# Performance work log

Hardware: AMD Instinct MI355X
Metric: run time of the kernel (lower is better)

Reference implementation:

```python
import jax, jax.numpy as jnp
import numpy as np

N = 100000      # nodes
E = 1200000     # edges (avg degree ~12)
D_IN = 64
D_OUT = 64


def setup_inputs() -> dict:
    key = jax.random.key(0)
    k1, k2, k3, k4 = jax.random.split(key, 4)
    x = jax.random.normal(k1, (N, D_IN), dtype=jnp.float32)
    # learned params (glorot-ish init)
    W = jax.random.normal(k2, (D_IN, D_OUT), dtype=jnp.float32) / np.sqrt(D_IN).astype(np.float32)
    b = jnp.zeros((D_OUT,), dtype=jnp.float32)
    src = jax.random.randint(k3, (E,), 0, N, dtype=jnp.int32)
    dst = jax.random.randint(k4, (E,), 0, N, dtype=jnp.int32)
    return {"x": x, "W": W, "b": b, "src": src, "dst": dst}


def reference(x, W, b, src, dst):
    # GCN layer: h = relu( D^-1/2 A D^-1/2 (x @ W) + b ), dropout=0 (eval)
    ones = jnp.ones(src.shape[0], dtype=x.dtype)
    deg_out = jax.ops.segment_sum(ones, src, num_segments=N)   # out-degree of source nodes
    deg_in = jax.ops.segment_sum(ones, dst, num_segments=N)    # in-degree of dest nodes
    norm_src = jax.lax.rsqrt(jnp.maximum(deg_out, 1.0))
    norm_dst = jax.lax.rsqrt(jnp.maximum(deg_in, 1.0))

    h = x @ W                                                  # [N, D_OUT] dense transform
    msg = h[src] * norm_src[src][:, None]                      # [E, D_OUT] gathered, pre-normalized messages
    agg = jax.ops.segment_sum(msg, dst, num_segments=N)        # [N, D_OUT] sparse aggregation
    out = agg * norm_dst[:, None] + b
    return jax.nn.relu(out)
```

## Files before the change

kernel.cpp:

```cpp
#include <hip/hip_runtime.h>
#include <hip/hip_bf16.h>

#define N_NODES 100000
#define N_EDGES 1200000
#define NPAIRS  (N_EDGES / 2)
#define DCH 64

#define K1B 256
#define K1T 1024
#define NRID 8
#define RID_NODES 12500
#define RID_WORDS 3125
#define SLICE_PAIRS (NPAIRS / (K1B / NRID))
#define SCAT_PAIRS ((NPAIRS + K1B - 1) / K1B)

#define BNODES 128
#define KBUK ((N_NODES + BNODES - 1) / BNODES)
#define CAPE 3008
#define CAPN 40

#define K2B 256
#define K2T 1024
#define GW_TOT (K2B * K2T / 64)

#define K3T 512

#define OFF_DEG      0
#define OFF_GCUR     100096
#define OFF_FLAG     103296
#define OFF_ESORT    103424
#define OFF_HS       9512704

__device__ __forceinline__ float load_f(const void* p, int i, int f32) {
    if (f32) return ((const float*)p)[i];
    return __bfloat162float(((const __hip_bfloat16*)p)[i]);
}

__device__ __forceinline__ unsigned short f2bf_bits(float f) {
    __hip_bfloat16 h = __float2bfloat16(f);
    return __builtin_bit_cast(unsigned short, h);
}

__global__ __launch_bounds__(K1T, 4)
void edges_kernel(const int* __restrict__ src,
                  const int* __restrict__ dst,
                  const void* __restrict__ x,
                  unsigned int* __restrict__ deg_packed,
                  int* __restrict__ gcur,
                  unsigned int* __restrict__ esort,
                  int* __restrict__ flag) {
    __shared__ unsigned int h[RID_WORDS];
    __shared__ int cnt[KBUK];
    __shared__ int base[KBUK];
    __shared__ int cur[KBUK];
    int tid = threadIdx.x, bid = blockIdx.x;

    if (bid == 0) {
        if (tid == 0) h[0] = 0;
        __syncthreads();
        if (tid < 256) {
            const unsigned short* u = (const unsigned short*)x;
            int c = 0;
            for (int i = tid * 16; i < tid * 16 + 16; ++i) {
                unsigned short v = u[2 * i];
                int e = (v >> 7) & 0xFF;
                if (e >= 141) c++;
            }
            if (c) atomicAdd(&h[0], (unsigned int)c);
        }
        __syncthreads();
        if (tid == 0) *flag = (h[0] > 256) ? 1 : 0;
        __syncthreads();
    }

    {
        int rid = bid & (NRID - 1);
        int j   = bid >> 3;
        for (int w = tid; w < RID_WORDS; w += K1T) h[w] = 0;
        __syncthreads();
        int lo = rid * RID_NODES;
        const int2* s2 = (const int2*)src;
        int p0 = j * SLICE_PAIRS, p1 = p0 + SLICE_PAIRS;
        for (int p = p0 + tid; p < p1; p += K1T) {
            int2 sp = s2[p];
            int n0 = sp.x - lo, n1 = sp.y - lo;
            if ((unsigned)n0 < (unsigned)RID_NODES)
                atomicAdd(&h[n0 >> 2], 1u << ((n0 & 3) * 8));
            if ((unsigned)n1 < (unsigned)RID_NODES)
                atomicAdd(&h[n1 >> 2], 1u << ((n1 & 3) * 8));
        }
        __syncthreads();
        unsigned int* dp = deg_packed + rid * RID_WORDS;
        for (int w = tid; w < RID_WORDS; w += K1T) {
            unsigned int v = h[w];
            if (v) atomicAdd(&dp[w], v);
        }
    }

    {
        int p0 = bid * SCAT_PAIRS;
        int p1 = p0 + SCAT_PAIRS; if (p1 > NPAIRS) p1 = NPAIRS;
        const int2* s2 = (const int2*)src;
        const int2* d2 = (const int2*)dst;
        for (int i = tid; i < KBUK; i += K1T) { cnt[i] = 0; cur[i] = 0; }
        __syncthreads();
        for (int p = p0 + tid; p < p1; p += K1T) {
            int2 dp = d2[p];
            atomicAdd(&cnt[dp.x >> 7], 1);
            atomicAdd(&cnt[dp.y >> 7], 1);
        }
        __syncthreads();
        for (int i = tid; i < KBUK; i += K1T)
            if (cnt[i]) base[i] = atomicAdd(&gcur[i], cnt[i]);
        __syncthreads();
        for (int p = p0 + tid; p < p1; p += K1T) {
            int2 sp = s2[p];
            int2 dp = d2[p];
            int b0 = dp.x >> 7, b1 = dp.y >> 7;
            int pos0 = base[b0] + atomicAdd(&cur[b0], 1);
            if (pos0 < CAPE)
                esort[b0 * CAPE + pos0] =
                    (unsigned int)sp.x | ((unsigned int)(dp.x & 127) << 24);
            int pos1 = base[b1] + atomicAdd(&cur[b1], 1);
            if (pos1 < CAPE)
                esort[b1 * CAPE + pos1] =
                    (unsigned int)sp.y | ((unsigned int)(dp.y & 127) << 24);
        }
    }
}

__global__ __launch_bounds__(K2T, 4)
void gemm_kernel(const void* __restrict__ x,
                 const void* __restrict__ W,
                 const unsigned int* __restrict__ deg_packed,
                 __hip_bfloat16* __restrict__ hs) {
    __shared__ float wt[DCH * 68];
    __shared__ int sn;
    int tid = threadIdx.x, bid = blockIdx.x;

    if (tid == 0) sn = 0;
    __syncthreads();
    if (tid < 256) {
        const unsigned short* u = (const unsigned short*)x;
        int c = 0;
        for (int i = tid * 16; i < tid * 16 + 16; ++i) {
            unsigned short v = u[2 * i];
            int e = (v >> 7) & 0xFF;
            if (e >= 141) c++;
        }
        if (c) atomicAdd(&sn, c);
    }
    __syncthreads();
    int f32 = sn > 256;

    for (int i = tid; i < DCH * DCH; i += K2T) {
        int kk = i >> 6, cc = i & 63;
        wt[cc * 68 + kk] = load_f(W, i, f32);
    }
    __syncthreads();

    int lane = tid & 63;
    const float4* wrow = (const float4*)(wt + lane * 68);
    float wr[DCH];
#pragma unroll
    for (int kq = 0; kq < 16; ++kq) {
        float4 t = wrow[kq];
        wr[4 * kq + 0] = t.x; wr[4 * kq + 1] = t.y;
        wr[4 * kq + 2] = t.z; wr[4 * kq + 3] = t.w;
    }
#pragma unroll
    for (int kk = 0; kk < DCH; ++kk)
        asm volatile("" : "+v"(wr[kk]));

    int gw = (bid << 4) + (tid >> 6);
#define RLA(i) __int_as_float(__builtin_amdgcn_readlane(xiA, (i)))
#define RLB(i) __int_as_float(__builtin_amdgcn_readlane(xiB, (i)))
#define GRP(j) \
    a0 = fmaf(RLA(4*(j)+0), wr[4*(j)+0], a0); \
    a1 = fmaf(RLA(4*(j)+1), wr[4*(j)+1], a1); \
    a2 = fmaf(RLA(4*(j)+2), wr[4*(j)+2], a2); \
    a3 = fmaf(RLA(4*(j)+3), wr[4*(j)+3], a3); \
    c0 = fmaf(RLB(4*(j)+0), wr[4*(j)+0], c0); \
    c1 = fmaf(RLB(4*(j)+1), wr[4*(j)+1], c1); \
    c2 = fmaf(RLB(4*(j)+2), wr[4*(j)+2], c2); \
    c3 = fmaf(RLB(4*(j)+3), wr[4*(j)+3], c3);

    for (int node = gw; node < N_NODES; node += 2 * GW_TOT) {
        int nodeB = node + GW_TOT;
        int hasB = nodeB < N_NODES;
        float xvA = load_f(x, node * DCH + lane, f32);
        float xvB = hasB ? load_f(x, nodeB * DCH + lane, f32) : 0.0f;
        int xiA = __float_as_int(xvA);
        int xiB = __float_as_int(xvB);
        float a0 = 0.f, a1 = 0.f, a2 = 0.f, a3 = 0.f;
        float c0 = 0.f, c1 = 0.f, c2 = 0.f, c3 = 0.f;
        GRP(0)  GRP(1)  GRP(2)  GRP(3)
        GRP(4)  GRP(5)  GRP(6)  GRP(7)
        GRP(8)  GRP(9)  GRP(10) GRP(11)
        GRP(12) GRP(13) GRP(14) GRP(15)
        unsigned int dwA = deg_packed[node >> 2];
        float dgA = (float)((dwA >> ((node & 3) * 8)) & 0xFFu);
        float nrA = rsqrtf(fmaxf(dgA, 1.0f));
        hs[node * DCH + lane] = __float2bfloat16(((a0 + a1) + (a2 + a3)) * nrA);
        if (hasB) {
            unsigned int dwB = deg_packed[nodeB >> 2];
            float dgB = (float)((dwB >> ((nodeB & 3) * 8)) & 0xFFu);
            float nrB = rsqrtf(fmaxf(dgB, 1.0f));
            hs[nodeB * DCH + lane] = __float2bfloat16(((c0 + c1) + (c2 + c3)) * nrB);
        }
    }
#undef RLA
#undef RLB
#undef GRP
}

__global__ __launch_bounds__(K3T, 6)
void gather_kernel(const __hip_bfloat16* __restrict__ hs,
                   const unsigned int* __restrict__ esort,
                   const int* __restrict__ gcur,
                   const void* __restrict__ b,
                   const int* __restrict__ flag,
                   void* __restrict__ out) {
    __shared__ unsigned int slots[BNODES * CAPN];
    __shared__ int cur[BNODES];
    int k = blockIdx.x, tid = threadIdx.x;
    int bbase = k * CAPE;
    int m = gcur[k];
    if (m > CAPE) m = CAPE;

    if (tid < BNODES) cur[tid] = 0;
    __syncthreads();
    for (int e = tid; e < m; e += K3T) {
        unsigned int w = esort[bbase + e];
        int r = w >> 24;
        int pos = atomicAdd(&cur[r], 1);
        if (pos < CAPN) slots[r * CAPN + pos] = w & 0xFFFFFFu;
    }
    __syncthreads();

    int f32 = *flag;
    int lane = tid & 63, wv = tid >> 6;
    int q = lane >> 4;
    int cg = lane & 15;
    const unsigned short* hsu = (const unsigned short*)hs;
    float b0 = load_f(b, cg * 4 + 0, f32);
    float b1 = load_f(b, cg * 4 + 1, f32);
    float b2 = load_f(b, cg * 4 + 2, f32);
    float b3 = load_f(b, cg * 4 + 3, f32);
    int nlo = k * BNODES;

#define ACC(ACCV, U) \
    (ACCV).x += __uint_as_float((U).x << 16); \
    (ACCV).y += __uint_as_float((U).x & 0xFFFF0000u); \
    (ACCV).z += __uint_as_float((U).y << 16); \
    (ACCV).w += __uint_as_float((U).y & 0xFFFF0000u);

    for (int base = wv; base < BNODES; base += 16) {
        int tA = base, tB = base + 8;
        int degA = cur[tA], degB = cur[tB];
        int dA = degA < CAPN ? degA : CAPN;
        int dB = degB < CAPN ? degB : CAPN;
        const unsigned int* eA = slots + tA * CAPN;
        const unsigned int* eB = slots + tB * CAPN;
        float4 aA0 = {0.f,0.f,0.f,0.f}, aA1 = {0.f,0.f,0.f,0.f};
        float4 aA2 = {0.f,0.f,0.f,0.f}, aA3 = {0.f,0.f,0.f,0.f};
        float4 aB0 = {0.f,0.f,0.f,0.f}, aB1 = {0.f,0.f,0.f,0.f};
        float4 aB2 = {0.f,0.f,0.f,0.f}, aB3 = {0.f,0.f,0.f,0.f};
        int dmax = dA > dB ? dA : dB;
        for (int j0 = 0; j0 < dmax; j0 += 16) {
            int i0 = j0 + q, i1 = j0 + 4 + q, i2 = j0 + 8 + q, i3 = j0 + 12 + q;
            unsigned int sA0 = (i0 < dA) ? eA[i0] : 0u;
            unsigned int sA1 = (i1 < dA) ? eA[i1] : 0u;
            unsigned int sA2 = (i2 < dA) ? eA[i2] : 0u;
            unsigned int sA3 = (i3 < dA) ? eA[i3] : 0u;
            unsigned int sB0 = (i0 < dB) ? eB[i0] : 0u;
            unsigned int sB1 = (i1 < dB) ? eB[i1] : 0u;
            unsigned int sB2 = (i2 < dB) ? eB[i2] : 0u;
            unsigned int sB3 = (i3 < dB) ? eB[i3] : 0u;
            uint2 uA0 = ((const uint2*)(hsu + sA0 * DCH))[cg];
            uint2 uA1 = ((const uint2*)(hsu + sA1 * DCH))[cg];
            uint2 uA2 = ((const uint2*)(hsu + sA2 * DCH))[cg];
            uint2 uA3 = ((const uint2*)(hsu + sA3 * DCH))[cg];
            uint2 uB0 = ((const uint2*)(hsu + sB0 * DCH))[cg];
            uint2 uB1 = ((const uint2*)(hsu + sB1 * DCH))[cg];
            uint2 uB2 = ((const uint2*)(hsu + sB2 * DCH))[cg];
            uint2 uB3 = ((const uint2*)(hsu + sB3 * DCH))[cg];
            if (i0 < dA) { ACC(aA0, uA0) }
            if (i1 < dA) { ACC(aA1, uA1) }
            if (i2 < dA) { ACC(aA2, uA2) }
            if (i3 < dA) { ACC(aA3, uA3) }
            if (i0 < dB) { ACC(aB0, uB0) }
            if (i1 < dB) { ACC(aB1, uB1) }
            if (i2 < dB) { ACC(aB2, uB2) }
            if (i3 < dB) { ACC(aB3, uB3) }
        }
        float4 oA, oB;
        oA.x = (aA0.x + aA1.x) + (aA2.x + aA3.x);
        oA.y = (aA0.y + aA1.y) + (aA2.y + aA3.y);
        oA.z = (aA0.z + aA1.z) + (aA2.z + aA3.z);
        oA.w = (aA0.w + aA1.w) + (aA2.w + aA3.w);
        oB.x = (aB0.x + aB1.x) + (aB2.x + aB3.x);
        oB.y = (aB0.y + aB1.y) + (aB2.y + aB3.y);
        oB.z = (aB0.z + aB1.z) + (aB2.z + aB3.z);
        oB.w = (aB0.w + aB1.w) + (aB2.w + aB3.w);
        oA.x += __shfl_xor(oA.x, 16); oA.y += __shfl_xor(oA.y, 16);
        oA.z += __shfl_xor(oA.z, 16); oA.w += __shfl_xor(oA.w, 16);
        oA.x += __shfl_xor(oA.x, 32); oA.y += __shfl_xor(oA.y, 32);
        oA.z += __shfl_xor(oA.z, 32); oA.w += __shfl_xor(oA.w, 32);
        oB.x += __shfl_xor(oB.x, 16); oB.y += __shfl_xor(oB.y, 16);
        oB.z += __shfl_xor(oB.z, 16); oB.w += __shfl_xor(oB.w, 16);
        oB.x += __shfl_xor(oB.x, 32); oB.y += __shfl_xor(oB.y, 32);
        oB.z += __shfl_xor(oB.z, 32); oB.w += __shfl_xor(oB.w, 32);
        int myNode = nlo + ((lane < 16) ? tA : tB);
        int myDeg  = (lane < 16) ? degA : degB;
        float4 o   = (lane < 16) ? oA : oB;
        if (lane < 32 && myNode < N_NODES) {
            float nrm = rsqrtf(fmaxf((float)myDeg, 1.0f));
            o.x = fmaxf(o.x * nrm + b0, 0.0f);
            o.y = fmaxf(o.y * nrm + b1, 0.0f);
            o.z = fmaxf(o.z * nrm + b2, 0.0f);
            o.w = fmaxf(o.w * nrm + b3, 0.0f);
            if (f32) {
                ((float4*)out)[myNode * 16 + cg] = o;
            } else {
                ushort4 s;
                s.x = f2bf_bits(o.x);
                s.y = f2bf_bits(o.y);
                s.z = f2bf_bits(o.z);
                s.w = f2bf_bits(o.w);
                ((ushort4*)out)[myNode * 16 + cg] = s;
            }
        }
    }
#undef ACC
}

extern "C" void kernel_launch(void* const* d_in, const int* in_sizes, int n_in,
                              void* d_out, int out_size, void* d_ws, size_t ws_size,
                              hipStream_t stream) {
    const void* x   = d_in[0];
    const void* W   = d_in[1];
    const void* b   = d_in[2];
    const int*  src = (const int*)d_in[3];
    const int*  dst = (const int*)d_in[4];

    char* ws = (char*)d_ws;
    unsigned int* deg_packed = (unsigned int*)(ws + OFF_DEG);
    int* gcur     = (int*)(ws + OFF_GCUR);
    int* flag     = (int*)(ws + OFF_FLAG);
    unsigned int* esort = (unsigned int*)(ws + OFF_ESORT);
    __hip_bfloat16* hs  = (__hip_bfloat16*)(ws + OFF_HS);

    (void)hipMemsetAsync(ws, 0, OFF_FLAG + 4, stream);

    edges_kernel<<<K1B, K1T, 0, stream>>>(
        src, dst, x, deg_packed, gcur, esort, flag);

    gemm_kernel<<<K2B, K2T, 0, stream>>>(x, W, deg_packed, hs);

    gather_kernel<<<KBUK, K3T, 0, stream>>>(hs, esort, gcur, b, flag, d_out);
}
```

Before: 178.7 us.

## Compute dense x@W transform with bf16 MFMA 16x16x32 tiles

Replaces the per-node readlane/FMA scalar GEMM with bf16 MFMA instructions over 16-node tiles, holding W fragments in registers as bf16. x is loaded with vector loads, converted to bf16 when it is f32, and fed to four column tiles. The launch shape also changes to 128 blocks of 512 threads. It trades fp32 accumulation inputs for bf16 inputs, which loses some precision, to cut ALU work in the transform stage. The GEMM is only one part of the pipeline, since scatter and gather kernels also run.

```diff
diff --git a/kernel.cpp b/kernel.cpp
--- a/kernel.cpp
+++ b/kernel.cpp
@@ -5,6 +5,9 @@
 #define N_EDGES 1200000
 #define NPAIRS  (N_EDGES / 2)
 #define DCH 64
+
+typedef __attribute__((ext_vector_type(8))) short bf16x8;
+typedef __attribute__((ext_vector_type(4))) float f32x4;
 
 #define K1B 256
 #define K1T 1024
@@ -19,9 +22,10 @@
 #define CAPE 3008
 #define CAPN 40
 
-#define K2B 256
-#define K2T 1024
-#define GW_TOT (K2B * K2T / 64)
+#define K2B 128
+#define K2T 512
+#define NTILES (N_NODES / 16)
+#define K2WAVES (K2B * K2T / 64)
 
 #define K3T 512
 
@@ -134,7 +138,7 @@
                  const void* __restrict__ W,
                  const unsigned int* __restrict__ deg_packed,
                  __hip_bfloat16* __restrict__ hs) {
-    __shared__ float wt[DCH * 68];
+    __shared__ float wt[DCH * DCH];
     __shared__ int sn;
     int tid = threadIdx.x, bid = blockIdx.x;
 
@@ -153,65 +157,76 @@
     __syncthreads();
     int f32 = sn > 256;
 
-    for (int i = tid; i < DCH * DCH; i += K2T) {
-        int kk = i >> 6, cc = i & 63;
-        wt[cc * 68 + kk] = load_f(W, i, f32);
-    }
+    for (int i = tid; i < DCH * DCH; i += K2T)
+        wt[i] = load_f(W, i, f32);
     __syncthreads();
 
     int lane = tid & 63;
-    const float4* wrow = (const float4*)(wt + lane * 68);
-    float wr[DCH];
+    int cB = lane & 15;
+    int k0 = (lane >> 4) * 8;
+
+    bf16x8 bf00, bf01, bf10, bf11, bf20, bf21, bf30, bf31;
+#define LDB(DST, CT, KH) { bf16x8 t;                                      \
+    _Pragma("unroll")                                                     \
+    for (int j = 0; j < 8; ++j)                                           \
+        t[j] = (short)f2bf_bits(wt[((KH)*32 + k0 + j) * DCH + (CT)*16 + cB]); \
+    DST = t; }
+    LDB(bf00, 0, 0) LDB(bf01, 0, 1)
+    LDB(bf10, 1, 0) LDB(bf11, 1, 1)
+    LDB(bf20, 2, 0) LDB(bf21, 2, 1)
+    LDB(bf30, 3, 0) LDB(bf31, 3, 1)
+#undef LDB
+
+    int wid = bid * (K2T / 64) + (tid >> 6);
+    int rowA = lane & 15;
+    for (int t = wid; t < NTILES; t += K2WAVES) {
+        int nbase = t << 4;
+        int node = nbase + rowA;
+        bf16x8 a0, a1;
+        if (f32) {
+            const float* xr = (const float*)x + node * DCH + k0;
+            float4 p0 = *(const float4*)(xr);
+            float4 p1 = *(const float4*)(xr + 4);
+            float4 p2 = *(const float4*)(xr + 32);
+            float4 p3 = *(const float4*)(xr + 36);
+            a0[0] = (short)f2bf_bits(p0.x); a0[1] = (short)f2bf_bits(p0.y);
+            a0[2] = (short)f2bf_bits(p0.z); a0[3] = (short)f2bf_bits(p0.w);
+            a0[4] = (short)f2bf_bits(p1.x); a0[5] = (short)f2bf_bits(p1.y);
+            a0[6] = (short)f2bf_bits(p1.z); a0[7] = (short)f2bf_bits(p1.w);
+            a1[0] = (short)f2bf_bits(p2.x); a1[1] = (short)f2bf_bits(p2.y);
+            a1[2] = (short)f2bf_bits(p2.z); a1[3] = (short)f2bf_bits(p2.w);
+            a1[4] = (short)f2bf_bits(p3.x); a1[5] = (short)f2bf_bits(p3.y);
+            a1[6] = (short)f2bf_bits(p3.z); a1[7] = (short)f2bf_bits(p3.w);
+        } else {
+            const short* xr = (const short*)x + node * DCH + k0;
+            a0 = *(const bf16x8*)(xr);
+            a1 = *(const bf16x8*)(xr + 32);
+        }
+        f32x4 ac0 = {0.f,0.f,0.f,0.f}, ac1 = {0.f,0.f,0.f,0.f};
+        f32x4 ac2 = {0.f,0.f,0.f,0.f}, ac3 = {0.f,0.f,0.f,0.f};
+        ac0 = __builtin_amdgcn_mfma_f32_16x16x32_bf16(a0, bf00, ac0, 0, 0, 0);
+        ac1 = __builtin_amdgcn_mfma_f32_16x16x32_bf16(a0, bf10, ac1, 0, 0, 0);
+        ac2 = __builtin_amdgcn_mfma_f32_16x16x32_bf16(a0, bf20, ac2, 0, 0, 0);
+        ac3 = __builtin_amdgcn_mfma_f32_16x16x32_bf16(a0, bf30, ac3, 0, 0, 0);
+        ac0 = __builtin_amdgcn_mfma_f32_16x16x32_bf16(a1, bf01, ac0, 0, 0, 0);
+        ac1 = __builtin_amdgcn_mfma_f32_16x16x32_bf16(a1, bf11, ac1, 0, 0, 0);
+        ac2 = __builtin_amdgcn_mfma_f32_16x16x32_bf16(a1, bf21, ac2, 0, 0, 0);
+        ac3 = __builtin_amdgcn_mfma_f32_16x16x32_bf16(a1, bf31, ac3, 0, 0, 0);
+
+        int rbase = nbase + (lane >> 4) * 4;
 #pragma unroll
-    for (int kq = 0; kq < 16; ++kq) {
-        float4 t = wrow[kq];
-        wr[4 * kq + 0] = t.x; wr[4 * kq + 1] = t.y;
-        wr[4 * kq + 2] = t.z; wr[4 * kq + 3] = t.w;
-    }
-#pragma unroll
-    for (int kk = 0; kk < DCH; ++kk)
-        asm volatile("" : "+v"(wr[kk]));
-
-    int gw = (bid << 4) + (tid >> 6);
-#define RLA(i) __int_as_float(__builtin_amdgcn_readlane(xiA, (i)))
-#define RLB(i) __int_as_float(__builtin_amdgcn_readlane(xiB, (i)))
-#define GRP(j) \
-    a0 = fmaf(RLA(4*(j)+0), wr[4*(j)+0], a0); \
-    a1 = fmaf(RLA(4*(j)+1), wr[4*(j)+1], a1); \
-    a2 = fmaf(RLA(4*(j)+2), wr[4*(j)+2], a2); \
-    a3 = fmaf(RLA(4*(j)+3), wr[4*(j)+3], a3); \
-    c0 = fmaf(RLB(4*(j)+0), wr[4*(j)+0], c0); \
-    c1 = fmaf(RLB(4*(j)+1), wr[4*(j)+1], c1); \
-    c2 = fmaf(RLB(4*(j)+2), wr[4*(j)+2], c2); \
-    c3 = fmaf(RLB(4*(j)+3), wr[4*(j)+3], c3);
-
-    for (int node = gw; node < N_NODES; node += 2 * GW_TOT) {
-        int nodeB = node + GW_TOT;
-        int hasB = nodeB < N_NODES;
-        float xvA = load_f(x, node * DCH + lane, f32);
-        float xvB = hasB ? load_f(x, nodeB * DCH + lane, f32) : 0.0f;
-        int xiA = __float_as_int(xvA);
-        int xiB = __float_as_int(xvB);
-        float a0 = 0.f, a1 = 0.f, a2 = 0.f, a3 = 0.f;
-        float c0 = 0.f, c1 = 0.f, c2 = 0.f, c3 = 0.f;
-        GRP(0)  GRP(1)  GRP(2)  GRP(3)
-        GRP(4)  GRP(5)  GRP(6)  GRP(7)
-        GRP(8)  GRP(9)  GRP(10) GRP(11)
-        GRP(12) GRP(13) GRP(14) GRP(15)
-        unsigned int dwA = deg_packed[node >> 2];
-        float dgA = (float)((dwA >> ((node & 3) * 8)) & 0xFFu);
-        float nrA = rsqrtf(fmaxf(dgA, 1.0f));
-        hs[node * DCH + lane] = __float2bfloat16(((a0 + a1) + (a2 + a3)) * nrA);
-        if (hasB) {
-            unsigned int dwB = deg_packed[nodeB >> 2];
-            float dgB = (float)((dwB >> ((nodeB & 3) * 8)) & 0xFFu);
-            float nrB = rsqrtf(fmaxf(dgB, 1.0f));
-            hs[nodeB * DCH + lane] = __float2bfloat16(((c0 + c1) + (c2 + c3)) * nrB);
-        }
-    }
-#undef RLA
-#undef RLB
-#undef GRP
+        for (int r = 0; r < 4; ++r) {
+            int n = rbase + r;
+            unsigned int dw = deg_packed[n >> 2];
+            float dg = (float)((dw >> ((n & 3) * 8)) & 0xFFu);
+            float nr = rsqrtf(fmaxf(dg, 1.0f));
+            __hip_bfloat16* ho = hs + n * DCH + cB;
+            ho[0]  = __float2bfloat16(ac0[r] * nr);
+            ho[16] = __float2bfloat16(ac1[r] * nr);
+            ho[32] = __float2bfloat16(ac2[r] * nr);
+            ho[48] = __float2bfloat16(ac3[r] * nr);
+        }
+    }
 }
 
 __global__ __launch_bounds__(K3T, 6)
```

After: 165.6 us. 7.3% less time.
